# Kernel optimization log

Measured on AMD Instinct MI355X. Metric: run time of the kernel, lower is better.

Reference implementation:

```python
import jax, jax.numpy as jnp
import numpy as np

N, E, IN, H, O, ED = 20000, 100000, 167, 4, 256, 10
HID = H * O  # 1024
BN_EPS = 1e-5


def _bn(x, g, b):
    # BatchNorm1d in training mode: batch statistics over nodes
    mu = x.mean(0)
    var = x.var(0)
    return (x - mu) * jax.lax.rsqrt(var + BN_EPS) * g + b


def _gat(x, src, dst, ef, Wg, We, attn, at, cb, heads, out):
    # modified_GAT: multi-head attention with edge features + time scalar
    n = x.shape[0]
    h = (x @ Wg).reshape(n, heads, out)                 # [N,H,O]
    e = (ef[:, 1:] @ We).reshape(-1, heads, out)        # [E,H,O] edge-feature proj
    t = ef[:, 0]                                        # [E] time feature
    # node-level attention scores (avoids materializing [E,H,O] twice)
    s_src = jnp.einsum('nhd,hd->nh', h, attn[0])
    s_dst = jnp.einsum('nhd,hd->nh', h, attn[1])
    s_e = jnp.einsum('ehd,hd->eh', e, attn[2])
    logits = jax.nn.leaky_relu(s_src[src] + s_dst[dst] + s_e + t[:, None] * at, 0.2)  # [E,H]
    # attention normalization: softmax over incoming edges of each dst node
    m = jax.ops.segment_max(logits, dst, num_segments=n)
    m = jnp.where(jnp.isfinite(m), m, 0.0)
    p = jnp.exp(logits - m[dst])
    denom = jax.ops.segment_sum(p, dst, num_segments=n)
    w = p / (denom[dst] + 1e-16)                        # [E,H]
    msg = w[:, :, None] * (h[src] + e)                  # [E,H,O]
    agg = jax.ops.segment_sum(msg, dst, num_segments=n) # [N,H,O]
    return agg.reshape(n, heads * out) + cb


def setup_inputs() -> dict:
    key = jax.random.key(0)
    ks = iter(jax.random.split(key, 64))

    def nrm(shape, s):
        return jax.random.normal(next(ks), shape, dtype=jnp.float32) * np.float32(s)

    d = {}
    d['x'] = jax.random.normal(next(ks), (N, IN), dtype=jnp.float32)
    d['edge_index'] = jax.random.randint(next(ks), (2, E), 0, N)
    d['edge_attr'] = jax.random.uniform(next(ks), (E, ED + 2), dtype=jnp.float32)
    conv_dims = [(IN, H, O), (HID, H, O), (HID, 1, 2)]
    for i, (fin, hh, oo) in enumerate(conv_dims, 1):
        d[f'Wg{i}'] = nrm((fin, hh * oo), 1.0 / np.sqrt(fin))
        d[f'We{i}'] = nrm((ED, hh * oo), 1.0 / np.sqrt(ED))
        d[f'attn{i}'] = nrm((3, hh, oo), 0.1)
        d[f'at{i}'] = nrm((hh,), 0.1)
        d[f'cb{i}'] = jnp.zeros((hh * oo,), jnp.float32)
    lin_dims = [(IN, HID), (HID, HID), (HID, 2)]
    bn_dims = [IN, HID, HID]
    for i, (fin, fo) in enumerate(lin_dims, 1):
        d[f'lw{i}'] = nrm((fin, fo), 1.0 / np.sqrt(fin))
        d[f'lb{i}'] = jnp.zeros((fo,), jnp.float32)
        d[f'g{i}'] = jnp.ones((bn_dims[i - 1],), jnp.float32)
        d[f'b{i}'] = jnp.zeros((bn_dims[i - 1],), jnp.float32)
    return d


def reference(x, edge_index, edge_attr,
              Wg1, We1, attn1, at1, cb1, lw1, lb1, g1, b1,
              Wg2, We2, attn2, at2, cb2, lw2, lb2, g2, b2,
              Wg3, We3, attn3, at3, cb3, lw3, lb3, g3, b3):
    src, dst = edge_index[0], edge_index[1]
    ef = edge_attr[:, :-1]  # drop edge class column
    h = _bn(x, g1, b1)
    h = jax.nn.relu(h @ lw1 + lb1 + _gat(h, src, dst, ef, Wg1, We1, attn1, at1, cb1, H, O))
    h = _bn(h, g2, b2)
    h = jax.nn.relu(h @ lw2 + lb2 + _gat(h, src, dst, ef, Wg2, We2, attn2, at2, cb2, H, O))
    h = _bn(h, g3, b3)
    h = jax.nn.relu(h @ lw3 + lb3 + _gat(h, src, dst, ef, Wg3, We3, attn3, at3, cb3, 1, 2))
    return h
```

## Files before the change

kernel.cpp:

```cpp
#include <hip/hip_runtime.h>
#include <math.h>

#define NN 20000
#define EE 100000
#define FIN 167
#define KP1 192
#define HID 1024
#define OO 256
#define NB 8

typedef unsigned short u16;
typedef short bf16x8 __attribute__((ext_vector_type(8)));
typedef short s16x4  __attribute__((ext_vector_type(4)));
typedef float f32x4  __attribute__((ext_vector_type(4)));

__device__ __forceinline__ float bf(u16 u){ return __uint_as_float(((unsigned)u)<<16); }
__device__ __forceinline__ u16 fb(float v){
  unsigned u = __float_as_uint(v);
  return (u16)((u + 0x7FFFu + ((u>>16)&1u)) >> 16);
}
__device__ __forceinline__ float ldv(const float* p, long i){ return p[i]; }
__device__ __forceinline__ float ldv(const u16*   p, long i){ return bf(p[i]); }

__global__ void k_count(const int* __restrict__ ei, int* __restrict__ counts){
  int e = blockIdx.x*256 + threadIdx.x;
  if (e < EE) atomicAdd(&counts[ei[EE+e]], 1);
}

__global__ __launch_bounds__(256) void k_scanA(const int* __restrict__ counts,
                                               int* __restrict__ iptr, int* __restrict__ bsum){
  __shared__ int sd[256];
  int b = blockIdx.x, tid = threadIdx.x;
  int i = b*256 + tid;
  int v = (i<NN)? counts[i] : 0;
  sd[tid]=v; __syncthreads();
  for (int off=1; off<256; off<<=1){
    int t = (tid>=off)? sd[tid-off] : 0;
    __syncthreads();
    sd[tid] += t;
    __syncthreads();
  }
  if (i<NN) iptr[i] = sd[tid]-v;
  if (tid==255) bsum[b]=sd[255];
}
__global__ __launch_bounds__(128) void k_scanB(const int* __restrict__ bsum,
                                               int* __restrict__ boff, int* __restrict__ iptrN,
                                               int nb){
  __shared__ int sd[128];
  int tid=threadIdx.x;
  int v=(tid<nb)? bsum[tid]:0;
  sd[tid]=v; __syncthreads();
  for (int off=1; off<128; off<<=1){
    int t=(tid>=off)?sd[tid-off]:0;
    __syncthreads();
    sd[tid]+=t;
    __syncthreads();
  }
  if (tid<nb) boff[tid]=sd[tid]-v;
  if (tid==127) *iptrN = sd[127];
}
__global__ void k_scanC(const int* __restrict__ boff, int* __restrict__ iptr){
  int i = blockIdx.x*256+threadIdx.x;
  if (i<NN) iptr[i] += boff[blockIdx.x];
}

__global__ void k_fill(const int* __restrict__ ei, const int* __restrict__ iptr,
                       int* __restrict__ cursor, int* __restrict__ eid){
  int e = blockIdx.x*256 + threadIdx.x;
  if (e < EE){
    int d = ei[EE+e];
    int pos = atomicAdd(&cursor[d],1);
    eid[iptr[d]+pos] = e;
  }
}

template<typename T>
__global__ void k_bnstats(const T* __restrict__ X, float* __restrict__ sums, int F){
  int f = blockIdx.y*256 + threadIdx.x;
  if (f >= F) return;
  int r0 = blockIdx.x*100, r1 = r0+100;
  float s=0.f, s2=0.f;
  for (int r=r0;r<r1;r++){ float v = ldv(X,(long)r*F+f); s += v; s2 += v*v; }
  atomicAdd(&sums[f], s);
  atomicAdd(&sums[F+f], s2);
}

__global__ __launch_bounds__(256) void k_bnstats8(const u16* __restrict__ X, float* __restrict__ part){
  int tid = threadIdx.x;
  int f8 = (tid & 127)*8;
  int r0 = blockIdx.x*79, r1 = min(NN, r0+79);
  float s[8]={0,0,0,0,0,0,0,0}, s2[8]={0,0,0,0,0,0,0,0};
  for (int r=r0 + (tid>>7); r<r1; r+=2){
    bf16x8 v = *(const bf16x8*)(X + (long)r*HID + f8);
    #pragma unroll
    for (int j=0;j<8;j++){ float x=bf((u16)v[j]); s[j]+=x; s2[j]+=x*x; }
  }
  __shared__ float red[256][8];
  float* pb = part + (long)blockIdx.x*2048;
  #pragma unroll
  for (int j=0;j<8;j++) red[tid][j]=s[j];
  __syncthreads();
  if (tid<128){
    #pragma unroll
    for (int j=0;j<8;j++) pb[f8+j] = red[tid][j]+red[tid+128][j];
  }
  __syncthreads();
  #pragma unroll
  for (int j=0;j<8;j++) red[tid][j]=s2[j];
  __syncthreads();
  if (tid<128){
    #pragma unroll
    for (int j=0;j<8;j++) pb[1024+f8+j] = red[tid][j]+red[tid+128][j];
  }
}

__global__ __launch_bounds__(256) void k_pred(const float* __restrict__ part, float* __restrict__ sums){
  int idx = blockIdx.x*256 + threadIdx.x;
  float s = 0.f;
  #pragma unroll 8
  for (int b=0;b<256;b++) s += part[(long)b*2048 + idx];
  sums[idx] = s;
}

__global__ void k_bnfin(const float* __restrict__ sums, const float* __restrict__ g,
                        const float* __restrict__ b, float* __restrict__ scale,
                        float* __restrict__ shift, int F){
  int f = blockIdx.x*256 + threadIdx.x;
  if (f >= F) return;
  float mu  = sums[f]   * (1.f/NN);
  float var = sums[F+f] * (1.f/NN) - mu*mu;
  float sc  = rsqrtf(var + 1e-5f) * g[f];
  scale[f] = sc;
  shift[f] = b[f] - mu*sc;
}

__global__ __launch_bounds__(256) void k_foldT(const float* __restrict__ Wg, const float* __restrict__ Wl,
                        const float* __restrict__ scale,
                        u16* __restrict__ Wt, int K, int Kp){
  __shared__ float t[32][33];
  int k0 = blockIdx.x*32, c0 = blockIdx.y*32;
  int tx = threadIdx.x & 31, ty = threadIdx.x >> 5;
  bool second = (c0 >= HID);
  const float* W = second ? Wl : Wg;
  int cc0 = second ? c0 - HID : c0;
  #pragma unroll
  for (int i=0;i<4;i++){
    int k = k0 + ty + i*8;
    t[ty+i*8][tx] = (k < K) ? W[(long)k*HID + cc0 + tx] * scale[k] : 0.f;
  }
  __syncthreads();
  #pragma unroll
  for (int i=0;i<4;i++){
    int c = c0 + ty + i*8;
    Wt[(long)c*Kp + k0 + tx] = fb(t[tx][ty+i*8]);
  }
}

__global__ void k_cinit(const float* __restrict__ lb, float* __restrict__ cst){
  int c = blockIdx.x*256 + threadIdx.x;
  if (c < 2*HID) cst[c] = (c >= HID) ? lb[c-HID] : 0.f;
}

__global__ __launch_bounds__(256) void k_const(const float* __restrict__ Wg, const float* __restrict__ Wl,
                        const float* __restrict__ shift, float* __restrict__ cst, int K){
  int tx = threadIdx.x & 63, ty = threadIdx.x >> 6;
  int c = blockIdx.x*64 + tx;
  bool second = c >= HID;
  const float* W = second ? Wl : Wg;
  int cc = second ? c-HID : c;
  int k0 = blockIdx.y*128;
  int k1 = min(K, k0+128);
  float s = 0.f;
  for (int k=k0+ty; k<k1; k+=4) s += shift[k]*W[(long)k*HID+cc];
  __shared__ float red[256];
  red[threadIdx.x] = s;
  __syncthreads();
  if (ty == 0){
    float tot = red[tx] + red[tx+64] + red[tx+128] + red[tx+192];
    atomicAdd(&cst[c], tot);
  }
}

__global__ void k_cast(const float* __restrict__ x, u16* __restrict__ xb){
  long idx = (long)blockIdx.x*256 + threadIdx.x;
  if (idx >= (long)NN*KP1) return;
  int n = (int)(idx / KP1), k = (int)(idx % KP1);
  xb[idx] = (k<FIN)? fb(x[(long)n*FIN+k]) : (u16)0;
}

__global__ void k_we16(const float* __restrict__ We, u16* __restrict__ We16){
  int i = blockIdx.x*256 + threadIdx.x;
  if (i < 10*HID) We16[i] = fb(We[i]);
}

#define MF(a_,b_,c_) __builtin_amdgcn_mfma_f32_16x16x32_bf16(a_,b_,c_,0,0,0)
#define FENCE asm volatile("" ::: "memory")
#define BAR do { FENCE; __builtin_amdgcn_s_barrier(); FENCE; } while(0)

__global__ __launch_bounds__(512,2) void k_gemm(const u16* __restrict__ A, int K,
                     const u16* __restrict__ Wt, const float* __restrict__ cst,
                     u16* __restrict__ Chg, u16* __restrict__ Clin){
  __shared__ u16 lds[3][12288];
  int b = blockIdx.x;
  int wg = (b & 7)*158 + (b >> 3);
  int row0 = (wg >> 4)*256, col0 = (wg & 15)*128;
  int tid = threadIdx.x;
  int wave = tid >> 6, lane = tid & 63, quad = lane >> 4, lo = lane & 15;
  int wm = wave >> 1, wn = wave & 1;
  const u16* Apt[2];
  #pragma unroll
  for (int i=0;i<2;i++){
    int s = i*512 + tid, srow = s>>2;
    int gr = row0 + srow; if (gr >= NN) gr = NN-1;
    Apt[i] = A + (long)gr*K + (((s&3)^((srow>>1)&3))*8);
  }
  int brow = tid>>2;
  const u16* Bpt = Wt + (long)(col0 + brow)*K + ((((tid&3)^((brow>>1)&3)))*8);
  const char* ldsc = (const char*)&lds[0][0];
  int axor = (lo>>1) & 3;
  int aoff = (wm*64 + lo)*64 + ((quad^axor)*16);
  int boff = 16384 + (wn*64 + lo)*64 + ((quad^axor)*16);
  int NT = K >> 5;
  f32x4 acc[4][4] = {};
  {
    u16* d0 = (u16*)&lds[0][0];
    u16* d1 = (u16*)&lds[1][0];
    __builtin_amdgcn_global_load_lds(Apt[0],      d0 +         tid*8, 16, 0, 0);
    __builtin_amdgcn_global_load_lds(Apt[1],      d0 + 4096 +  tid*8, 16, 0, 0);
    __builtin_amdgcn_global_load_lds(Bpt,         d0 + 8192 +  tid*8, 16, 0, 0);
    __builtin_amdgcn_global_load_lds(Apt[0] + 32, d1 +         tid*8, 16, 0, 0);
    __builtin_amdgcn_global_load_lds(Apt[1] + 32, d1 + 4096 +  tid*8, 16, 0, 0);
    __builtin_amdgcn_global_load_lds(Bpt    + 32, d1 + 8192 +  tid*8, 16, 0, 0);
    asm volatile("s_waitcnt vmcnt(3)" ::: "memory");
    BAR;
  }
  int cb = 0;
  for (int t=0; t<NT; t++){
    const char* Lb = ldsc + cb*24576;
    bf16x8 af[4], bfr[4];
    #pragma unroll
    for (int i=0;i<4;i++) af[i]  = *(const bf16x8*)(Lb + aoff + i*1024);
    #pragma unroll
    for (int n=0;n<4;n++) bfr[n] = *(const bf16x8*)(Lb + boff + n*1024);
    int nx2 = (t+2 < NT);
    if (nx2){
      int sb = cb+2; if (sb>=3) sb-=3;
      u16* Sd = (u16*)&lds[0][0] + sb*12288;
      int ko = (t+2) << 5;
      __builtin_amdgcn_global_load_lds(Apt[0] + ko, Sd +         tid*8, 16, 0, 0);
      __builtin_amdgcn_global_load_lds(Apt[1] + ko, Sd + 4096 +  tid*8, 16, 0, 0);
      __builtin_amdgcn_global_load_lds(Bpt    + ko, Sd + 8192 +  tid*8, 16, 0, 0);
    }
    #pragma unroll
    for (int i=0;i<4;i++)
      #pragma unroll
      for (int n=0;n<4;n++)
        acc[i][n] = MF(af[i], bfr[n], acc[i][n]);
    if (t+1 < NT){
      if (nx2) asm volatile("s_waitcnt vmcnt(3)" ::: "memory");
      else     asm volatile("s_waitcnt vmcnt(0)" ::: "memory");
      BAR;
    }
    cb++; if (cb>=3) cb=0;
  }
  #pragma unroll
  for (int i=0;i<4;i++){
    #pragma unroll
    for (int n=0;n<4;n++){
      int col = col0 + wn*64 + n*16 + lo;
      float cs = cst[col];
      #pragma unroll
      for (int r=0;r<4;r++){
        int row = row0 + wm*64 + i*16 + quad*4 + r;
        if (row < NN){
          u16 o = fb(acc[i][n][r] + cs);
          if (col < HID) Chg[(long)row*HID + col] = o;
          else           Clin[(long)row*HID + col - HID] = o;
        }
      }
    }
  }
}
#undef MF
#undef BAR
#undef FENCE

__global__ __launch_bounds__(256) void k_sdot(const u16* __restrict__ hg, const float* __restrict__ attn,
                       float* __restrict__ ssrc, float* __restrict__ sdst){
  int unit = blockIdx.x*4 + (threadIdx.x >> 6);
  if (unit >= NN*4) return;
  int lane = threadIdx.x & 63;
  int n = unit >> 2, h = unit & 3;
  const u16* hp = hg + (long)n*HID + h*OO + lane*4;
  s16x4 v = *(const s16x4*)hp;
  float4 x0 = *(const float4*)(attn + h*OO + lane*4);
  float4 x1 = *(const float4*)(attn + HID + h*OO + lane*4);
  float f0 = bf((u16)v.x), f1 = bf((u16)v.y), f2 = bf((u16)v.z), f3 = bf((u16)v.w);
  float ss = f0*x0.x + f1*x0.y + f2*x0.z + f3*x0.w;
  float sd = f0*x1.x + f1*x1.y + f2*x1.z + f3*x1.w;
  #pragma unroll
  for (int off=32; off>0; off>>=1){
    ss += __shfl_down(ss, off);
    sd += __shfl_down(sd, off);
  }
  if (lane==0){ ssrc[unit]=ss; sdst[unit]=sd; }
}

__global__ void k_q(const float* __restrict__ We, const float* __restrict__ attn,
                    float* __restrict__ q){
  int t = threadIdx.x;
  if (t >= 40) return;
  int k = t >> 2, h = t & 3;
  float s = 0.f;
  for (int d=0; d<OO; d++) s += We[(long)k*HID + h*OO + d] * attn[2*HID + h*OO + d];
  q[k*4+h] = s;
}

__global__ void k_logits(const int* __restrict__ ei, const float* __restrict__ ea,
                         const float* __restrict__ q, const float* __restrict__ at,
                         const float* __restrict__ ssrc, const float* __restrict__ sdst,
                         float* __restrict__ L){
  int e = blockIdx.x*256 + threadIdx.x;
  if (e >= EE) return;
  int s = ei[e], dd = ei[EE+e];
  float4 a0 = *(const float4*)(ea + (long)e*12);
  float4 a1 = *(const float4*)(ea + (long)e*12 + 4);
  float4 a2 = *(const float4*)(ea + (long)e*12 + 8);
  float t = a0.x;
  float cc[10] = {a0.y,a0.z,a0.w, a1.x,a1.y,a1.z,a1.w, a2.x,a2.y,a2.z};
  float4 ss = *(const float4*)(ssrc + (long)s*4);
  float4 sd = *(const float4*)(sdst + (long)dd*4);
  float sv[4] = {ss.x+sd.x, ss.y+sd.y, ss.z+sd.z, ss.w+sd.w};
  float4 out;
  #pragma unroll
  for (int h=0;h<4;h++){
    float se = 0.f;
    #pragma unroll
    for (int k=0;k<10;k++) se += cc[k]*q[k*4+h];
    float v = sv[h] + se + t*at[h];
    ((float*)&out)[h] = (v>0.f)? v : 0.2f*v;
  }
  *(float4*)(L + (long)e*4) = out;
}

__global__ __launch_bounds__(128) void k_mden(const int* __restrict__ iptr, const int* __restrict__ eid,
                       const float* __restrict__ ea, float* __restrict__ L,
                       float* __restrict__ cw, float* __restrict__ dv4){
  int n = blockIdx.x*128 + threadIdx.x;
  if (n >= NN) return;
  int b = iptr[n], e1 = iptr[n+1];
  float m0=-INFINITY, m1=-INFINITY, m2=-INFINITY, m3=-INFINITY;
  for (int i=b;i<e1;i++){
    float4 l = *(const float4*)(L + (long)eid[i]*4);
    m0=fmaxf(m0,l.x); m1=fmaxf(m1,l.y); m2=fmaxf(m2,l.z); m3=fmaxf(m3,l.w);
  }
  if (b==e1){ m0=m1=m2=m3=0.f; }
  float s0=0.f,s1=0.f,s2=0.f,s3=0.f;
  float c[4][10] = {};
  for (int i=b;i<e1;i++){
    int e = eid[i];
    float4 l = *(const float4*)(L + (long)e*4);
    float4 p = { expf(l.x-m0), expf(l.y-m1), expf(l.z-m2), expf(l.w-m3) };
    *(float4*)(L + (long)e*4) = p;
    s0+=p.x; s1+=p.y; s2+=p.z; s3+=p.w;
    float4 a0 = *(const float4*)(ea + (long)e*12);
    float4 a1 = *(const float4*)(ea + (long)e*12 + 4);
    float4 a2 = *(const float4*)(ea + (long)e*12 + 8);
    float cc[10] = {a0.y,a0.z,a0.w, a1.x,a1.y,a1.z,a1.w, a2.x,a2.y,a2.z};
    #pragma unroll
    for (int k=0;k<10;k++){
      c[0][k] += p.x*cc[k]; c[1][k] += p.y*cc[k];
      c[2][k] += p.z*cc[k]; c[3][k] += p.w*cc[k];
    }
  }
  float d0=1.f/(s0+1e-16f), d1=1.f/(s1+1e-16f), d2=1.f/(s2+1e-16f), d3=1.f/(s3+1e-16f);
  float* cp = cw + (long)n*40;
  #pragma unroll
  for (int k=0;k<10;k++){
    cp[k]    = c[0][k]*d0;
    cp[10+k] = c[1][k]*d1;
    cp[20+k] = c[2][k]*d2;
    cp[30+k] = c[3][k]*d3;
  }
  float4 dv = {d0,d1,d2,d3};
  *(float4*)(dv4 + (long)n*4) = dv;
}

__global__ __launch_bounds__(256) void k_gath(
    const u16* __restrict__ hg, const int* __restrict__ ei,
    const int* __restrict__ iptr, const int* __restrict__ eid,
    const float* __restrict__ L,
    const float* __restrict__ cw,
    const float* __restrict__ dv4,
    const u16* __restrict__ We16, const float* __restrict__ cb,
    u16* __restrict__ lio)
{
  __shared__ u16  sWe[10*HID];
  __shared__ float scb[HID];
  int tid = threadIdx.x;
  for (int i=tid;i<10*HID;i+=256) sWe[i] = We16[i];
  for (int i=tid;i<HID;i+=256) scb[i] = cb[i];
  __syncthreads();
  int h = tid >> 6;
  int f0 = tid*4;
  int d0 = blockIdx.x*NB, dend = min(NN, d0+NB);
  for (int d=d0; d<dend; d++){
    s16x4 a0 = *(const s16x4*)(lio + (long)d*HID + f0);
    float acc0=bf((u16)a0.x), acc1=bf((u16)a0.y), acc2=bf((u16)a0.z), acc3=bf((u16)a0.w);
    float gt0=0.f, gt1=0.f, gt2=0.f, gt3=0.f;
    float dv = dv4[(long)d*4 + h];
    int b0 = iptr[d], en = iptr[d+1];
    float wN = 0.f; s16x4 vN = {};
    if (b0 < en){
      int e = eid[b0], s_ = ei[e];
      wN = L[(long)e*4 + h];
      vN = *(const s16x4*)(hg + (long)s_*HID + f0);
    }
    for (int i=b0;i<en;i++){
      float w = wN; s16x4 v = vN;
      if (i+1 < en){
        int e2 = eid[i+1], s2 = ei[e2];
        wN = L[(long)e2*4 + h];
        vN = *(const s16x4*)(hg + (long)s2*HID + f0);
      }
      gt0 += w*bf((u16)v.x); gt1 += w*bf((u16)v.y);
      gt2 += w*bf((u16)v.z); gt3 += w*bf((u16)v.w);
    }
    acc0 += dv*gt0; acc1 += dv*gt1; acc2 += dv*gt2; acc3 += dv*gt3;
    const float* cp = cw + (long)d*40 + h*10;
    float ew0=0.f, ew1=0.f, ew2=0.f, ew3=0.f;
    #pragma unroll
    for (int k=0;k<10;k++){
      float c = cp[k];
      s16x4 wv = *(const s16x4*)(sWe + k*HID + f0);
      ew0 += c*bf((u16)wv.x); ew1 += c*bf((u16)wv.y);
      ew2 += c*bf((u16)wv.z); ew3 += c*bf((u16)wv.w);
    }
    acc0 += ew0; acc1 += ew1; acc2 += ew2; acc3 += ew3;
    u16 o[4];
    o[0] = fb(fmaxf(acc0 + scb[f0  ], 0.f));
    o[1] = fb(fmaxf(acc1 + scb[f0+1], 0.f));
    o[2] = fb(fmaxf(acc2 + scb[f0+2], 0.f));
    o[3] = fb(fmaxf(acc3 + scb[f0+3], 0.f));
    *(s16x4*)(lio + (long)d*HID + f0) = *(const s16x4*)o;
  }
}

__global__ void k_c4init(const float* __restrict__ lb, float* __restrict__ c4){
  if (threadIdx.x==0 && blockIdx.x==0){ c4[0]=0.f; c4[1]=0.f; c4[2]=lb[0]; c4[3]=lb[1]; }
}

__global__ __launch_bounds__(256) void k_fold3(const float* __restrict__ Wg, const float* __restrict__ lw,
                        const float* __restrict__ scale, const float* __restrict__ shift,
                        float* __restrict__ W4, float* __restrict__ c4){
  int k = blockIdx.x*256 + threadIdx.x;
  float sc = scale[k], sh = shift[k];
  float w0=Wg[k*2], w1=Wg[k*2+1], l0=lw[k*2], l1=lw[k*2+1];
  float4 o = {w0*sc, w1*sc, l0*sc, l1*sc};
  *(float4*)(W4 + (long)k*4) = o;
  __shared__ float red[256][4];
  int tid = threadIdx.x;
  red[tid][0]=sh*w0; red[tid][1]=sh*w1; red[tid][2]=sh*l0; red[tid][3]=sh*l1;
  __syncthreads();
  for (int o2=128;o2>0;o2>>=1){
    if (tid<o2){
      #pragma unroll
      for (int j=0;j<4;j++) red[tid][j]+=red[tid+o2][j];
    }
    __syncthreads();
  }
  if (tid==0){
    #pragma unroll
    for (int j=0;j<4;j++) atomicAdd(&c4[j], red[0][j]);
  }
}

__global__ __launch_bounds__(256) void k_n3(const u16* __restrict__ in,
    const float* __restrict__ W4, const float* __restrict__ c4,
    const float* __restrict__ attn,
    float* __restrict__ hg3, float* __restrict__ lin3,
    float* __restrict__ ssrc, float* __restrict__ sdst)
{
  __shared__ float sW[HID*4];
  __shared__ float sx[4][HID];
  int tid = threadIdx.x;
  int n0 = blockIdx.x*4;
  for (int i=tid; i<HID; i+=256) *(float4*)&sW[i*4] = *(const float4*)(W4 + (long)i*4);
  for (int idx=tid; idx<512; idx+=256){
    int rr = idx>>7, ch = idx&127;
    bf16x8 v = *(const bf16x8*)(in + (long)(n0+rr)*HID + ch*8);
    #pragma unroll
    for (int j=0;j<8;j++) sx[rr][ch*8+j] = bf((u16)v[j]);
  }
  __syncthreads();
  int w = tid>>6, lane = tid&63;
  float p0=0.f,p1=0.f,p2=0.f,p3=0.f;
  #pragma unroll
  for (int g=0; g<16; g++){
    int k = g*64 + lane;
    float x = sx[w][k];
    float4 wv = *(const float4*)&sW[k*4];
    p0 += x*wv.x; p1 += x*wv.y; p2 += x*wv.z; p3 += x*wv.w;
  }
  #pragma unroll
  for (int off=32; off>0; off>>=1){
    p0 += __shfl_down(p0, off);
    p1 += __shfl_down(p1, off);
    p2 += __shfl_down(p2, off);
    p3 += __shfl_down(p3, off);
  }
  if (lane==0){
    int n = n0 + w;
    float r0=p0+c4[0], r1=p1+c4[1], r2=p2+c4[2], r3=p3+c4[3];
    hg3[n*2]=r0; hg3[n*2+1]=r1;
    lin3[n*2]=r2; lin3[n*2+1]=r3;
    ssrc[n]=r0*attn[0]+r1*attn[1];
    sdst[n]=r0*attn[2]+r1*attn[3];
  }
}

__global__ void k_logits3(const int* __restrict__ ei, const float* __restrict__ ea,
                          const float* __restrict__ We, const float* __restrict__ attn,
                          const float* __restrict__ at, const float* __restrict__ ssrc,
                          const float* __restrict__ sdst, float* __restrict__ L){
  int e = blockIdx.x*256 + threadIdx.x;
  if (e >= EE) return;
  int s = ei[e], d = ei[EE+e];
  float e0=0.f, e1=0.f;
  #pragma unroll
  for (int k=0;k<10;k++){
    float c = ea[e*12+1+k];
    e0 += c*We[k*2]; e1 += c*We[k*2+1];
  }
  float se = e0*attn[4] + e1*attn[5];
  float v = ssrc[s] + sdst[d] + se + ea[e*12]*at[0];
  L[e] = (v>0.f)? v : 0.2f*v;
}

__global__ __launch_bounds__(128) void k_mden3(const int* __restrict__ iptr, const int* __restrict__ eid,
                        const float* __restrict__ ea, float* __restrict__ L,
                        float* __restrict__ cw, float* __restrict__ dvn){
  int n = blockIdx.x*128 + threadIdx.x;
  if (n >= NN) return;
  int b = iptr[n], e1 = iptr[n+1];
  float mx = -INFINITY;
  for (int i=b;i<e1;i++) mx = fmaxf(mx, L[eid[i]]);
  if (b == e1) mx = 0.f;
  float s = 0.f;
  float c[10] = {0.f,0.f,0.f,0.f,0.f,0.f,0.f,0.f,0.f,0.f};
  for (int i=b;i<e1;i++){
    int e = eid[i];
    float p = expf(L[e]-mx);
    L[e] = p;
    s += p;
    #pragma unroll
    for (int k=0;k<10;k++) c[k] += p*ea[e*12+1+k];
  }
  float dv = 1.f/(s+1e-16f);
  float* cp = cw + (long)n*10;
  #pragma unroll
  for (int k=0;k<10;k++) cp[k] = c[k]*dv;
  dvn[n] = dv;
}

__global__ __launch_bounds__(128) void k_gather3(const int* __restrict__ ei,
                          const int* __restrict__ iptr, const int* __restrict__ eid,
                          const float* __restrict__ L,
                          const float* __restrict__ cw,
                          const float* __restrict__ dvn,
                          const float* __restrict__ hg3,
                          const float* __restrict__ We, const float* __restrict__ lin3,
                          const float* __restrict__ cb, float* __restrict__ out){
  int n = blockIdx.x*128 + threadIdx.x;
  if (n >= NN) return;
  int b = iptr[n], en = iptr[n+1];
  const float* cp = cw + (long)n*10;
  float e0f=0.f, e1f=0.f;
  #pragma unroll
  for (int k=0;k<10;k++){ e0f += cp[k]*We[k*2]; e1f += cp[k]*We[k*2+1]; }
  float a0=0.f, a1=0.f;
  for (int i=b;i<en;i++){
    int e = eid[i], s_ = ei[e];
    float w = L[e];
    a0 += w*hg3[s_*2];
    a1 += w*hg3[s_*2+1];
  }
  float dv = dvn[n];
  out[n*2]   = fmaxf(lin3[n*2]  +dv*a0+e0f+cb[0], 0.f);
  out[n*2+1] = fmaxf(lin3[n*2+1]+dv*a1+e1f+cb[1], 0.f);
}

extern "C" void kernel_launch(void* const* d_in, const int* in_sizes, int n_in,
                              void* d_out, int out_size, void* d_ws, size_t ws_size,
                              hipStream_t stream){
  const int* ei = (const int*)d_in[1];

  long long sz[64];
  {
    const long long* s64 = (const long long*)(const void*)in_sizes;
    bool is64 = (n_in >= 2) && (in_sizes[0] == 3340000) && (in_sizes[1] == 0)
                && (s64[1] == 200000);
    for (int i=0;i<n_in && i<64;i++) sz[i] = is64 ? s64[i] : (long long)in_sizes[i];
  }

  int IWg[3], IWe[3], IAttn[3], IAt[3], ICb[3], ILw[3], ILb[3], IG[3], IB[3];
  if (n_in > 8 && sz[8] == (long long)HID*HID){
    for (int l=0;l<3;l++){
      IWg[l]=3+l*5; IWe[l]=4+l*5; IAttn[l]=5+l*5; IAt[l]=6+l*5; ICb[l]=7+l*5;
      ILw[l]=18+l*4; ILb[l]=19+l*4; IG[l]=20+l*4; IB[l]=21+l*4;
    }
  } else {
    int idx=3;
    for (int l=0;l<3;l++){
      IWg[l]=idx++; IWe[l]=idx++; IAttn[l]=idx++; IAt[l]=idx++; ICb[l]=idx++;
      ILw[l]=idx++; ILb[l]=idx++; IG[l]=idx++; IB[l]=idx++;
    }
  }
  #define FP(i) ((const float*)d_in[(i)])

  char* ws = (char*)d_ws;
  size_t off = 0;
  auto alloc = [&](size_t bytes)->void*{ void* p = ws + off; off += (bytes + 255) & ~(size_t)255; return p; };
  auto G = [](long n){ return (int)((n+255)/256); };

  u16*   buf0 = (u16*)  alloc((size_t)NN*HID*2);
  u16*   bufA = (u16*)  alloc((size_t)NN*HID*2);
  u16*   bufB = (u16*)  alloc((size_t)NN*HID*2);
  u16*   xbf  = (u16*)  alloc((size_t)NN*KP1*2);
  u16*   Wt   = (u16*)  alloc((size_t)2*HID*HID*2);
  u16*   We16 = (u16*)  alloc((size_t)10*HID*2);
  float* cst  = (float*)alloc(2*HID*4);
  float* L    = (float*)alloc((size_t)EE*4*4);
  float* ssrc = (float*)alloc((size_t)NN*4*4);
  float* sdst = (float*)alloc((size_t)NN*4*4);
  float* dv4  = (float*)alloc((size_t)NN*4*4);
  int*   iptr = (int*)  alloc((size_t)(NN+4)*4);
  int*   cnts = (int*)  alloc((size_t)NN*4);
  int*   eid  = (int*)  alloc((size_t)EE*4);
  int*   bsum = (int*)  alloc(256*4);
  int*   boff = (int*)  alloc(256*4);
  float* stats= (float*)alloc(2*HID*4);
  float* scale= (float*)alloc(HID*4);
  float* shift= (float*)alloc(HID*4);
  float* qbuf = (float*)alloc(64*4);
  float* hg3  = (float*)alloc((size_t)NN*2*4);
  float* lin3 = (float*)alloc((size_t)NN*2*4);
  float* cw   = (float*)alloc((size_t)NN*40*4);
  float* W4   = (float*)alloc((size_t)HID*4*4);
  float* c4   = (float*)alloc(4*4);
  float* part = (float*)alloc((size_t)256*2048*4);

  int nsb = G(NN);
  hipMemsetAsync(cnts, 0, NN*sizeof(int), stream);
  k_count<<<G(EE),256,0,stream>>>(ei, cnts);
  k_scanA<<<nsb,256,0,stream>>>(cnts, iptr, bsum);
  k_scanB<<<1,128,0,stream>>>(bsum, boff, iptr+NN, nsb);
  k_scanC<<<nsb,256,0,stream>>>(boff, iptr);
  hipMemsetAsync(cnts, 0, NN*sizeof(int), stream);
  k_fill<<<G(EE),256,0,stream>>>(ei, iptr, cnts, eid);

  int gg = 1264;
  int gsd = (NN*4+3)/4;
  int gnd = (NN+127)/128;

  {
    hipMemsetAsync(stats, 0, 2*FIN*sizeof(float), stream);
    dim3 bg(200, 1);
    k_bnstats<float><<<bg,256,0,stream>>>(FP(0), stats, FIN);
    k_bnfin<<<1,256,0,stream>>>(stats, FP(IG[0]), FP(IB[0]), scale, shift, FIN);
    k_cast<<<G((long)NN*KP1),256,0,stream>>>(FP(0), xbf);
    dim3 ft(KP1/32, 64);
    k_foldT<<<ft,256,0,stream>>>(FP(IWg[0]), FP(ILw[0]), scale, Wt, FIN, KP1);
    k_cinit<<<8,256,0,stream>>>(FP(ILb[0]), cst);
    dim3 cg(32, (FIN+127)/128);
    k_const<<<cg,256,0,stream>>>(FP(IWg[0]), FP(ILw[0]), shift, cst, FIN);
    k_we16<<<40,256,0,stream>>>(FP(IWe[0]), We16);
    k_gemm<<<gg,512,0,stream>>>(xbf, KP1, Wt, cst, buf0, bufA);
    k_sdot<<<gsd,256,0,stream>>>(buf0, FP(IAttn[0]), ssrc, sdst);
    k_q<<<1,64,0,stream>>>(FP(IWe[0]), FP(IAttn[0]), qbuf);
    k_logits<<<G(EE),256,0,stream>>>(ei, FP(2), qbuf, FP(IAt[0]), ssrc, sdst, L);
    k_mden<<<gnd,128,0,stream>>>(iptr, eid, FP(2), L, cw, dv4);
    k_gath<<<(NN+NB-1)/NB,256,0,stream>>>(buf0, ei, iptr, eid, L, cw, dv4,
                                          We16, FP(ICb[0]), bufA);
  }
  {
    k_bnstats8<<<256,256,0,stream>>>(bufA, part);
    k_pred<<<8,256,0,stream>>>(part, stats);
    k_bnfin<<<4,256,0,stream>>>(stats, FP(IG[1]), FP(IB[1]), scale, shift, HID);
    dim3 ft(HID/32, 64);
    k_foldT<<<ft,256,0,stream>>>(FP(IWg[1]), FP(ILw[1]), scale, Wt, HID, HID);
    k_cinit<<<8,256,0,stream>>>(FP(ILb[1]), cst);
    dim3 cg(32, HID/128);
    k_const<<<cg,256,0,stream>>>(FP(IWg[1]), FP(ILw[1]), shift, cst, HID);
    k_we16<<<40,256,0,stream>>>(FP(IWe[1]), We16);
    k_gemm<<<gg,512,0,stream>>>(bufA, HID, Wt, cst, buf0, bufB);
    k_sdot<<<gsd,256,0,stream>>>(buf0, FP(IAttn[1]), ssrc, sdst);
    k_q<<<1,64,0,stream>>>(FP(IWe[1]), FP(IAttn[1]), qbuf);
    k_logits<<<G(EE),256,0,stream>>>(ei, FP(2), qbuf, FP(IAt[1]), ssrc, sdst, L);
    k_mden<<<gnd,128,0,stream>>>(iptr, eid, FP(2), L, cw, dv4);
    k_gath<<<(NN+NB-1)/NB,256,0,stream>>>(buf0, ei, iptr, eid, L, cw, dv4,
                                          We16, FP(ICb[1]), bufB);
  }

  k_bnstats8<<<256,256,0,stream>>>(bufB, part);
  k_pred<<<8,256,0,stream>>>(part, stats);
  k_bnfin<<<4,256,0,stream>>>(stats, FP(IG[2]), FP(IB[2]), scale, shift, HID);
  k_c4init<<<1,64,0,stream>>>(FP(ILb[2]), c4);
  k_fold3<<<HID/256,256,0,stream>>>(FP(IWg[2]), FP(ILw[2]), scale, shift, W4, c4);
  k_n3<<<NN/4,256,0,stream>>>(bufB, W4, c4, FP(IAttn[2]), hg3, lin3, ssrc, sdst);
  k_logits3<<<G(EE),256,0,stream>>>(ei, FP(2), FP(IWe[2]), FP(IAttn[2]), FP(IAt[2]), ssrc, sdst, L);
  k_mden3<<<gnd,128,0,stream>>>(iptr, eid, FP(2), L, cw, dv4);
  k_gather3<<<gnd,128,0,stream>>>(ei, iptr, eid, L, cw, dv4, hg3,
                                  FP(IWe[2]), lin3, FP(ICb[2]), (float*)d_out);
}
```

Before: 732.3 us.

## Fuse edge logit computation into per-node softmax kernels and interleave two nodes in gather

Removes the separate per-edge logits kernels. Logits are now computed inside the per-destination max/denominator kernels (k_mden, k_mden3), which saves launches and one write-then-read pass over L. The gather kernel now handles two destination nodes at once with interleaved edge loops, so more independent loads are in flight. The guard on the final node block was removed; this is safe because NN is divisible by NB. The fused logit computation runs once per destination thread, which is less parallel than per-edge threads and may suffer load imbalance.

New measurement: 732.7 us. About the same (+0.1%).

```diff
diff --git a/kernel.cpp b/kernel.cpp
--- a/kernel.cpp
+++ b/kernel.cpp
@@ -316,43 +316,40 @@
   q[k*4+h] = s;
 }
 
-__global__ void k_logits(const int* __restrict__ ei, const float* __restrict__ ea,
-                         const float* __restrict__ q, const float* __restrict__ at,
-                         const float* __restrict__ ssrc, const float* __restrict__ sdst,
-                         float* __restrict__ L){
-  int e = blockIdx.x*256 + threadIdx.x;
-  if (e >= EE) return;
-  int s = ei[e], dd = ei[EE+e];
-  float4 a0 = *(const float4*)(ea + (long)e*12);
-  float4 a1 = *(const float4*)(ea + (long)e*12 + 4);
-  float4 a2 = *(const float4*)(ea + (long)e*12 + 8);
-  float t = a0.x;
-  float cc[10] = {a0.y,a0.z,a0.w, a1.x,a1.y,a1.z,a1.w, a2.x,a2.y,a2.z};
-  float4 ss = *(const float4*)(ssrc + (long)s*4);
-  float4 sd = *(const float4*)(sdst + (long)dd*4);
-  float sv[4] = {ss.x+sd.x, ss.y+sd.y, ss.z+sd.z, ss.w+sd.w};
-  float4 out;
-  #pragma unroll
-  for (int h=0;h<4;h++){
-    float se = 0.f;
-    #pragma unroll
-    for (int k=0;k<10;k++) se += cc[k]*q[k*4+h];
-    float v = sv[h] + se + t*at[h];
-    ((float*)&out)[h] = (v>0.f)? v : 0.2f*v;
-  }
-  *(float4*)(L + (long)e*4) = out;
-}
-
 __global__ __launch_bounds__(128) void k_mden(const int* __restrict__ iptr, const int* __restrict__ eid,
-                       const float* __restrict__ ea, float* __restrict__ L,
-                       float* __restrict__ cw, float* __restrict__ dv4){
+                       const int* __restrict__ ei, const float* __restrict__ ea,
+                       const float* __restrict__ q, const float* __restrict__ at,
+                       const float* __restrict__ ssrc, const float* __restrict__ sdst,
+                       float* __restrict__ L, float* __restrict__ cw, float* __restrict__ dv4){
   int n = blockIdx.x*128 + threadIdx.x;
   if (n >= NN) return;
   int b = iptr[n], e1 = iptr[n+1];
+  float4 sdv = *(const float4*)(sdst + (long)n*4);
+  float at0=at[0], at1=at[1], at2=at[2], at3=at[3];
   float m0=-INFINITY, m1=-INFINITY, m2=-INFINITY, m3=-INFINITY;
   for (int i=b;i<e1;i++){
-    float4 l = *(const float4*)(L + (long)eid[i]*4);
-    m0=fmaxf(m0,l.x); m1=fmaxf(m1,l.y); m2=fmaxf(m2,l.z); m3=fmaxf(m3,l.w);
+    int e = eid[i], s_ = ei[e];
+    float4 a0 = *(const float4*)(ea + (long)e*12);
+    float4 a1 = *(const float4*)(ea + (long)e*12 + 4);
+    float4 a2 = *(const float4*)(ea + (long)e*12 + 8);
+    float t = a0.x;
+    float cc[10] = {a0.y,a0.z,a0.w, a1.x,a1.y,a1.z,a1.w, a2.x,a2.y,a2.z};
+    float4 ss = *(const float4*)(ssrc + (long)s_*4);
+    float se0=0.f, se1=0.f, se2=0.f, se3=0.f;
+    #pragma unroll
+    for (int k=0;k<10;k++){
+      float c = cc[k];
+      se0 += c*q[k*4];   se1 += c*q[k*4+1];
+      se2 += c*q[k*4+2]; se3 += c*q[k*4+3];
+    }
+    float v0 = ss.x + sdv.x + se0 + t*at0;
+    float v1 = ss.y + sdv.y + se1 + t*at1;
+    float v2 = ss.z + sdv.z + se2 + t*at2;
+    float v3 = ss.w + sdv.w + se3 + t*at3;
+    float4 lg = { (v0>0.f)?v0:0.2f*v0, (v1>0.f)?v1:0.2f*v1,
+                  (v2>0.f)?v2:0.2f*v2, (v3>0.f)?v3:0.2f*v3 };
+    *(float4*)(L + (long)e*4) = lg;
+    m0=fmaxf(m0,lg.x); m1=fmaxf(m1,lg.y); m2=fmaxf(m2,lg.z); m3=fmaxf(m3,lg.w);
   }
   if (b==e1){ m0=m1=m2=m3=0.f; }
   float s0=0.f,s1=0.f,s2=0.f,s3=0.f;
@@ -403,46 +400,69 @@
   __syncthreads();
   int h = tid >> 6;
   int f0 = tid*4;
-  int d0 = blockIdx.x*NB, dend = min(NN, d0+NB);
-  for (int d=d0; d<dend; d++){
-    s16x4 a0 = *(const s16x4*)(lio + (long)d*HID + f0);
-    float acc0=bf((u16)a0.x), acc1=bf((u16)a0.y), acc2=bf((u16)a0.z), acc3=bf((u16)a0.w);
-    float gt0=0.f, gt1=0.f, gt2=0.f, gt3=0.f;
-    float dv = dv4[(long)d*4 + h];
-    int b0 = iptr[d], en = iptr[d+1];
-    float wN = 0.f; s16x4 vN = {};
-    if (b0 < en){
-      int e = eid[b0], s_ = ei[e];
-      wN = L[(long)e*4 + h];
-      vN = *(const s16x4*)(hg + (long)s_*HID + f0);
-    }
-    for (int i=b0;i<en;i++){
-      float w = wN; s16x4 v = vN;
-      if (i+1 < en){
-        int e2 = eid[i+1], s2 = ei[e2];
-        wN = L[(long)e2*4 + h];
-        vN = *(const s16x4*)(hg + (long)s2*HID + f0);
-      }
-      gt0 += w*bf((u16)v.x); gt1 += w*bf((u16)v.y);
-      gt2 += w*bf((u16)v.z); gt3 += w*bf((u16)v.w);
-    }
-    acc0 += dv*gt0; acc1 += dv*gt1; acc2 += dv*gt2; acc3 += dv*gt3;
-    const float* cp = cw + (long)d*40 + h*10;
-    float ew0=0.f, ew1=0.f, ew2=0.f, ew3=0.f;
+  int d0 = blockIdx.x*NB;
+  for (int d=d0; d<d0+NB; d+=2){
+    int dA = d, dB = d+1;
+    s16x4 iA4 = *(const s16x4*)(lio + (long)dA*HID + f0);
+    s16x4 iB4 = *(const s16x4*)(lio + (long)dB*HID + f0);
+    float aA0=bf((u16)iA4.x), aA1=bf((u16)iA4.y), aA2=bf((u16)iA4.z), aA3=bf((u16)iA4.w);
+    float aB0=bf((u16)iB4.x), aB1=bf((u16)iB4.y), aB2=bf((u16)iB4.z), aB3=bf((u16)iB4.w);
+    float gA0=0.f,gA1=0.f,gA2=0.f,gA3=0.f;
+    float gB0=0.f,gB1=0.f,gB2=0.f,gB3=0.f;
+    float dvA = dv4[(long)dA*4 + h];
+    float dvB = dv4[(long)dB*4 + h];
+    int bA=iptr[dA], eA=iptr[dA+1];
+    int bB=iptr[dB], eB=iptr[dB+1];
+    float wNA=0.f, wNB=0.f; s16x4 vNA={}, vNB={};
+    if (bA<eA){ int e=eid[bA], s_=ei[e]; wNA=L[(long)e*4+h]; vNA=*(const s16x4*)(hg+(long)s_*HID+f0); }
+    if (bB<eB){ int e=eid[bB], s_=ei[e]; wNB=L[(long)e*4+h]; vNB=*(const s16x4*)(hg+(long)s_*HID+f0); }
+    int iA=bA, iB=bB;
+    while (iA<eA && iB<eB){
+      float wA=wNA, wB=wNB; s16x4 vA=vNA, vB=vNB;
+      if (iA+1<eA){ int e2=eid[iA+1], s2=ei[e2]; wNA=L[(long)e2*4+h]; vNA=*(const s16x4*)(hg+(long)s2*HID+f0); }
+      if (iB+1<eB){ int e2=eid[iB+1], s2=ei[e2]; wNB=L[(long)e2*4+h]; vNB=*(const s16x4*)(hg+(long)s2*HID+f0); }
+      gA0 += wA*bf((u16)vA.x); gA1 += wA*bf((u16)vA.y);
+      gA2 += wA*bf((u16)vA.z); gA3 += wA*bf((u16)vA.w);
+      gB0 += wB*bf((u16)vB.x); gB1 += wB*bf((u16)vB.y);
+      gB2 += wB*bf((u16)vB.z); gB3 += wB*bf((u16)vB.w);
+      iA++; iB++;
+    }
+    while (iA<eA){
+      float wA=wNA; s16x4 vA=vNA;
+      if (iA+1<eA){ int e2=eid[iA+1], s2=ei[e2]; wNA=L[(long)e2*4+h]; vNA=*(const s16x4*)(hg+(long)s2*HID+f0); }
+      gA0 += wA*bf((u16)vA.x); gA1 += wA*bf((u16)vA.y);
+      gA2 += wA*bf((u16)vA.z); gA3 += wA*bf((u16)vA.w);
+      iA++;
+    }
+    while (iB<eB){
+      float wB=wNB; s16x4 vB=vNB;
+      if (iB+1<eB){ int e2=eid[iB+1], s2=ei[e2]; wNB=L[(long)e2*4+h]; vNB=*(const s16x4*)(hg+(long)s2*HID+f0); }
+      gB0 += wB*bf((u16)vB.x); gB1 += wB*bf((u16)vB.y);
+      gB2 += wB*bf((u16)vB.z); gB3 += wB*bf((u16)vB.w);
+      iB++;
+    }
+    aA0 += dvA*gA0; aA1 += dvA*gA1; aA2 += dvA*gA2; aA3 += dvA*gA3;
+    aB0 += dvB*gB0; aB1 += dvB*gB1; aB2 += dvB*gB2; aB3 += dvB*gB3;
+    const float* cpA = cw + (long)dA*40 + h*10;
+    const float* cpB = cw + (long)dB*40 + h*10;
+    float eA0=0.f,eA1=0.f,eA2=0.f,eA3=0.f;
+    float eB0=0.f,eB1=0.f,eB2=0.f,eB3=0.f;
     #pragma unroll
     for (int k=0;k<10;k++){
-      float c = cp[k];
       s16x4 wv = *(const s16x4*)(sWe + k*HID + f0);
-      ew0 += c*bf((u16)wv.x); ew1 += c*bf((u16)wv.y);
-      ew2 += c*bf((u16)wv.z); ew3 += c*bf((u16)wv.w);
-    }
-    acc0 += ew0; acc1 += ew1; acc2 += ew2; acc3 += ew3;
-    u16 o[4];
-    o[0] = fb(fmaxf(acc0 + scb[f0  ], 0.f));
-    o[1] = fb(fmaxf(acc1 + scb[f0+1], 0.f));
-    o[2] = fb(fmaxf(acc2 + scb[f0+2], 0.f));
-    o[3] = fb(fmaxf(acc3 + scb[f0+3], 0.f));
-    *(s16x4*)(lio + (long)d*HID + f0) = *(const s16x4*)o;
+      float w0=bf((u16)wv.x), w1=bf((u16)wv.y), w2=bf((u16)wv.z), w3=bf((u16)wv.w);
+      float cA = cpA[k], cB = cpB[k];
+      eA0 += cA*w0; eA1 += cA*w1; eA2 += cA*w2; eA3 += cA*w3;
+      eB0 += cB*w0; eB1 += cB*w1; eB2 += cB*w2; eB3 += cB*w3;
+    }
+    float b0=scb[f0], b1=scb[f0+1], b2=scb[f0+2], b3=scb[f0+3];
+    u16 oA[4], oB[4];
+    oA[0]=fb(fmaxf(aA0+eA0+b0,0.f)); oA[1]=fb(fmaxf(aA1+eA1+b1,0.f));
+    oA[2]=fb(fmaxf(aA2+eA2+b2,0.f)); oA[3]=fb(fmaxf(aA3+eA3+b3,0.f));
+    oB[0]=fb(fmaxf(aB0+eB0+b0,0.f)); oB[1]=fb(fmaxf(aB1+eB1+b1,0.f));
+    oB[2]=fb(fmaxf(aB2+eB2+b2,0.f)); oB[3]=fb(fmaxf(aB3+eB3+b3,0.f));
+    *(s16x4*)(lio + (long)dA*HID + f0) = *(const s16x4*)oA;
+    *(s16x4*)(lio + (long)dB*HID + f0) = *(const s16x4*)oB;
   }
 }
 
@@ -519,32 +539,31 @@
   }
 }
 
-__global__ void k_logits3(const int* __restrict__ ei, const float* __restrict__ ea,
-                          const float* __restrict__ We, const float* __restrict__ attn,
-                          const float* __restrict__ at, const float* __restrict__ ssrc,
-                          const float* __restrict__ sdst, float* __restrict__ L){
-  int e = blockIdx.x*256 + threadIdx.x;
-  if (e >= EE) return;
-  int s = ei[e], d = ei[EE+e];
-  float e0=0.f, e1=0.f;
-  #pragma unroll
-  for (int k=0;k<10;k++){
-    float c = ea[e*12+1+k];
-    e0 += c*We[k*2]; e1 += c*We[k*2+1];
-  }
-  float se = e0*attn[4] + e1*attn[5];
-  float v = ssrc[s] + sdst[d] + se + ea[e*12]*at[0];
-  L[e] = (v>0.f)? v : 0.2f*v;
-}
-
 __global__ __launch_bounds__(128) void k_mden3(const int* __restrict__ iptr, const int* __restrict__ eid,
-                        const float* __restrict__ ea, float* __restrict__ L,
-                        float* __restrict__ cw, float* __restrict__ dvn){
+                        const int* __restrict__ ei, const float* __restrict__ ea,
+                        const float* __restrict__ We, const float* __restrict__ attn,
+                        const float* __restrict__ at, const float* __restrict__ ssrc,
+                        const float* __restrict__ sdst,
+                        float* __restrict__ L, float* __restrict__ cw, float* __restrict__ dvn){
   int n = blockIdx.x*128 + threadIdx.x;
   if (n >= NN) return;
   int b = iptr[n], e1 = iptr[n+1];
+  float sdv = sdst[n];
+  float a4 = attn[4], a5 = attn[5], at0 = at[0];
   float mx = -INFINITY;
-  for (int i=b;i<e1;i++) mx = fmaxf(mx, L[eid[i]]);
+  for (int i=b;i<e1;i++){
+    int e = eid[i], s_ = ei[e];
+    float e0=0.f, e1v=0.f;
+    #pragma unroll
+    for (int k=0;k<10;k++){
+      float c = ea[e*12+1+k];
+      e0 += c*We[k*2]; e1v += c*We[k*2+1];
+    }
+    float v = ssrc[s_] + sdv + e0*a4 + e1v*a5 + ea[e*12]*at0;
+    float lg = (v>0.f)? v : 0.2f*v;
+    L[e] = lg;
+    mx = fmaxf(mx, lg);
+  }
   if (b == e1) mx = 0.f;
   float s = 0.f;
   float c[10] = {0.f,0.f,0.f,0.f,0.f,0.f,0.f,0.f,0.f,0.f};
@@ -678,8 +697,7 @@
     k_gemm<<<gg,512,0,stream>>>(xbf, KP1, Wt, cst, buf0, bufA);
     k_sdot<<<gsd,256,0,stream>>>(buf0, FP(IAttn[0]), ssrc, sdst);
     k_q<<<1,64,0,stream>>>(FP(IWe[0]), FP(IAttn[0]), qbuf);
-    k_logits<<<G(EE),256,0,stream>>>(ei, FP(2), qbuf, FP(IAt[0]), ssrc, sdst, L);
-    k_mden<<<gnd,128,0,stream>>>(iptr, eid, FP(2), L, cw, dv4);
+    k_mden<<<gnd,128,0,stream>>>(iptr, eid, ei, FP(2), qbuf, FP(IAt[0]), ssrc, sdst, L, cw, dv4);
     k_gath<<<(NN+NB-1)/NB,256,0,stream>>>(buf0, ei, iptr, eid, L, cw, dv4,
                                           We16, FP(ICb[0]), bufA);
   }
@@ -696,8 +714,7 @@
     k_gemm<<<gg,512,0,stream>>>(bufA, HID, Wt, cst, buf0, bufB);
     k_sdot<<<gsd,256,0,stream>>>(buf0, FP(IAttn[1]), ssrc, sdst);
     k_q<<<1,64,0,stream>>>(FP(IWe[1]), FP(IAttn[1]), qbuf);
-    k_logits<<<G(EE),256,0,stream>>>(ei, FP(2), qbuf, FP(IAt[1]), ssrc, sdst, L);
-    k_mden<<<gnd,128,0,stream>>>(iptr, eid, FP(2), L, cw, dv4);
+    k_mden<<<gnd,128,0,stream>>>(iptr, eid, ei, FP(2), qbuf, FP(IAt[1]), ssrc, sdst, L, cw, dv4);
     k_gath<<<(NN+NB-1)/NB,256,0,stream>>>(buf0, ei, iptr, eid, L, cw, dv4,
                                           We16, FP(ICb[1]), bufB);
   }
@@ -708,8 +725,8 @@
   k_c4init<<<1,64,0,stream>>>(FP(ILb[2]), c4);
   k_fold3<<<HID/256,256,0,stream>>>(FP(IWg[2]), FP(ILw[2]), scale, shift, W4, c4);
   k_n3<<<NN/4,256,0,stream>>>(bufB, W4, c4, FP(IAttn[2]), hg3, lin3, ssrc, sdst);
-  k_logits3<<<G(EE),256,0,stream>>>(ei, FP(2), FP(IWe[2]), FP(IAttn[2]), FP(IAt[2]), ssrc, sdst, L);
-  k_mden3<<<gnd,128,0,stream>>>(iptr, eid, FP(2), L, cw, dv4);
+  k_mden3<<<gnd,128,0,stream>>>(iptr, eid, ei, FP(2), FP(IWe[2]), FP(IAttn[2]), FP(IAt[2]),
+                                ssrc, sdst, L, cw, dv4);
   k_gather3<<<gnd,128,0,stream>>>(ei, iptr, eid, L, cw, dv4, hg3,
                                   FP(IWe[2]), lin3, FP(ICb[2]), (float*)d_out);
 }
```
